# Kernel tuning notes

Hardware: AMD Instinct MI355X
Metric: run time of the kernel (lower is better)

The kernel has to match this reference:

```python
import jax, jax.numpy as jnp
import numpy as np
from jax import lax


def setup_inputs() -> dict:
    key = jax.random.key(0)
    ks = jax.random.split(key, 6)
    B, T, F, C = 32, 256, 64, 16
    CO, P, S, K = 16, 64, 32, 4
    x = jax.random.normal(ks[0], (B, T, F, C), dtype=jnp.float32)
    static = jax.random.normal(ks[1], (B, S), dtype=jnp.float32)
    conv_w = jax.random.normal(ks[2], (F, CO, C, K), dtype=jnp.float32) * (1.0 / np.sqrt(C * K))
    conv_b = jax.random.normal(ks[3], (F, CO), dtype=jnp.float32) * 0.01
    W_p = jax.random.normal(ks[4], (F * C + S, P), dtype=jnp.float32) * (1.0 / np.sqrt(F * C + S))
    b_p = jax.random.normal(ks[5], (P,), dtype=jnp.float32) * 0.01
    return {"x": x, "static": static, "conv_w": conv_w, "conv_b": conv_b,
            "W_p": W_p, "b_p": b_p, "dilation": 2}


def _tpc_forward(x, static, conv_w, conv_b, W_p, b_p, dilation):
    B, T, F, C = x.shape
    _, CO, _, K = conv_w.shape
    left_pad = dilation * (K - 1)
    # --- feature-wise causal temporal conv as one grouped dilated conv ---
    # [B, T, F, C] -> [B, F*C, T]  (NCH layout)
    xr = x.transpose(0, 2, 3, 1).reshape(B, F * C, T)
    kr = conv_w.reshape(F * CO, C, K)  # groups = F
    y = lax.conv_general_dilated(
        xr, kr,
        window_strides=(1,),
        padding=[(left_pad, 0)],  # causal left padding
        rhs_dilation=(dilation,),
        dimension_numbers=("NCH", "OIH", "NCH"),
        feature_group_count=F,
    )  # [B, F*CO, T]
    temp_out = y.reshape(B, F, CO, T).transpose(0, 3, 1, 2) + conv_b[None, None, :, :]
    # --- pointwise branch on flattened features + static ---
    flat_x = x.reshape(B, T, F * C)
    static_rep = jnp.broadcast_to(static[:, None, :], (B, T, static.shape[-1]))
    point_in = jnp.concatenate([flat_x, static_rep], axis=-1)  # [B, T, F*C+S]
    point_out = point_in @ W_p + b_p  # [B, T, P]
    point_bcast = jnp.broadcast_to(point_out[:, :, None, :], (B, T, F, point_out.shape[-1]))
    # --- concat fusion + ReLU ---
    fused = jnp.concatenate([x, temp_out, point_bcast], axis=-1)
    return jax.nn.relu(fused)


def reference(x, static, conv_w, conv_b, W_p, b_p, dilation):
    return _tpc_forward(x, static, conv_w, conv_b, W_p, b_p, dilation)
```

## Files before the change

kernel.cpp:

```cpp
#include <hip/hip_runtime.h>

#define B_  32
#define T_  256
#define F_  64
#define C_  16
#define CO_ 16
#define P_  64
#define S_  32
#define K_  4
#define FC_ 1024
#define OUTC 96
#define TT  8
#define NS  14

__global__ __launch_bounds__(512, 4) void tpc_fused(
    const float* __restrict__ x, const float* __restrict__ stat,
    const float* __restrict__ cw, const float* __restrict__ cb,
    const float* __restrict__ Wp, const float* __restrict__ bp,
    float* __restrict__ out)
{
    __shared__ __align__(16) float xs[NS * FC_];
    __shared__ __align__(16) float u[4096];

    int tid = threadIdx.x;
    int blk = blockIdx.x;
    int b  = blk >> 5;
    int t0 = (blk & 31) * TT;

    #pragma unroll
    for (int it = 0; it < 7; ++it) {
        int v = it * 512 + tid;
        int slice = v >> 8;
        int pos   = v & 255;
        int tg = t0 - 6 + slice;
        float4 val = make_float4(0.f, 0.f, 0.f, 0.f);
        if (tg >= 0)
            val = *(const float4*)(x + ((size_t)(b * T_ + tg)) * FC_ + pos * 4);
        *(float4*)(xs + slice * FC_ + pos * 4) = val;
    }
    __syncthreads();

    {
        int p  = tid & 63;
        int ks = tid >> 6;
        float acc[TT];
        #pragma unroll
        for (int r = 0; r < TT; ++r) acc[r] = 0.f;
        int k0base = ks * 128;
        for (int kk = 0; kk < 128; kk += 4) {
            int k0 = k0base + kk;
            float w0 = Wp[(size_t)(k0 + 0) * P_ + p];
            float w1 = Wp[(size_t)(k0 + 1) * P_ + p];
            float w2 = Wp[(size_t)(k0 + 2) * P_ + p];
            float w3 = Wp[(size_t)(k0 + 3) * P_ + p];
            #pragma unroll
            for (int r = 0; r < TT; ++r) {
                float4 xv = *(const float4*)(xs + (6 + r) * FC_ + k0);
                acc[r] += xv.x * w0 + xv.y * w1 + xv.z * w2 + xv.w * w3;
            }
        }
        #pragma unroll
        for (int r = 0; r < TT; ++r)
            u[(ks * TT + r) * P_ + p] = acc[r];
    }
    __syncthreads();

    {
        int p = tid & 63;
        int r = tid >> 6;
        float s = bp[p];
        const float* wst = Wp + (size_t)FC_ * P_;
        #pragma unroll 8
        for (int si = 0; si < S_; ++si)
            s += stat[b * S_ + si] * wst[si * P_ + p];
        #pragma unroll
        for (int ks = 0; ks < 8; ++ks)
            s += u[(ks * TT + r) * P_ + p];
        __syncthreads();
        u[3072 + r * P_ + p] = fmaxf(s, 0.f);
    }
    __syncthreads();

    int co = tid & 15;
    int fh = tid >> 4;
    int p  = tid & 63;
    int fg = tid >> 6;

    #pragma unroll
    for (int half = 0; half < 2; ++half) {
        int f = half * 32 + fh;
        float w[64];
        const float4* wg = (const float4*)(cw + ((size_t)(f * CO_ + co)) * (C_ * K_));
        #pragma unroll
        for (int j = 0; j < 16; ++j) {
            float4 t4 = wg[j];
            w[4 * j + 0] = t4.x; w[4 * j + 1] = t4.y;
            w[4 * j + 2] = t4.z; w[4 * j + 3] = t4.w;
        }
        float bias = cb[f * CO_ + co];

        for (int tl = 0; tl < TT; ++tl) {
            float temp = bias;
            #pragma unroll
            for (int k = 0; k < K_; ++k) {
                const float* sp = xs + (tl + 2 * k) * FC_ + f * C_;
                #pragma unroll
                for (int c4 = 0; c4 < 4; ++c4) {
                    float4 xv = *(const float4*)(sp + c4 * 4);
                    temp += xv.x * w[(c4 * 4 + 0) * 4 + k];
                    temp += xv.y * w[(c4 * 4 + 1) * 4 + k];
                    temp += xv.z * w[(c4 * 4 + 2) * 4 + k];
                    temp += xv.w * w[(c4 * 4 + 3) * 4 + k];
                }
            }
            u[fh * OUTC + 16 + co] = fmaxf(temp, 0.f);
            u[fh * OUTC + co] = fmaxf(xs[(tl + 6) * FC_ + f * C_ + co], 0.f);
            float pvv = u[3072 + tl * P_ + p];
            #pragma unroll
            for (int fo = 0; fo < 4; ++fo)
                u[(fo * 8 + fg) * OUTC + 32 + p] = pvv;

            asm volatile("s_waitcnt lgkmcnt(0)" ::: "memory");
            __builtin_amdgcn_sched_barrier(0);
            __builtin_amdgcn_s_barrier();
            __builtin_amdgcn_sched_barrier(0);

            {
                const float4* src = (const float4*)u;
                float4* dst = (float4*)(out + ((size_t)(b * T_ + t0 + tl)) * F_ * OUTC
                                        + half * 3072);
                dst[tid] = src[tid];
                if (tid < 256) dst[512 + tid] = src[512 + tid];
            }

            asm volatile("s_waitcnt lgkmcnt(0)" ::: "memory");
            __builtin_amdgcn_sched_barrier(0);
            __builtin_amdgcn_s_barrier();
            __builtin_amdgcn_sched_barrier(0);
        }
    }
}

extern "C" void kernel_launch(void* const* d_in, const int* in_sizes, int n_in,
                              void* d_out, int out_size, void* d_ws, size_t ws_size,
                              hipStream_t stream) {
    const float* x    = (const float*)d_in[0];
    const float* stat = (const float*)d_in[1];
    const float* cw   = (const float*)d_in[2];
    const float* cb   = (const float*)d_in[3];
    const float* Wp   = (const float*)d_in[4];
    const float* bp   = (const float*)d_in[5];
    float* out = (float*)d_out;

    tpc_fused<<<1024, 512, 0, stream>>>(x, stat, cw, cb, Wp, bp, out);
}
```

Before: 280.2 us.

## Read x from global instead of LDS and double-buffer the output staging

```diff
diff --git a/kernel.cpp b/kernel.cpp
--- a/kernel.cpp
+++ b/kernel.cpp
@@ -11,7 +11,6 @@
 #define FC_ 1024
 #define OUTC 96
 #define TT  8
-#define NS  14
 
 __global__ __launch_bounds__(512, 4) void tpc_fused(
     const float* __restrict__ x, const float* __restrict__ stat,
@@ -19,26 +18,16 @@
     const float* __restrict__ Wp, const float* __restrict__ bp,
     float* __restrict__ out)
 {
-    __shared__ __align__(16) float xs[NS * FC_];
-    __shared__ __align__(16) float u[4096];
+    __shared__ __align__(16) float lds[6656];
+    float* part = lds;
+    float* pv   = lds + 6144;
 
     int tid = threadIdx.x;
     int blk = blockIdx.x;
     int b  = blk >> 5;
     int t0 = (blk & 31) * TT;
 
-    #pragma unroll
-    for (int it = 0; it < 7; ++it) {
-        int v = it * 512 + tid;
-        int slice = v >> 8;
-        int pos   = v & 255;
-        int tg = t0 - 6 + slice;
-        float4 val = make_float4(0.f, 0.f, 0.f, 0.f);
-        if (tg >= 0)
-            val = *(const float4*)(x + ((size_t)(b * T_ + tg)) * FC_ + pos * 4);
-        *(float4*)(xs + slice * FC_ + pos * 4) = val;
-    }
-    __syncthreads();
+    const float* xrow0 = x + ((size_t)(b * T_ + t0)) * FC_;
 
     {
         int p  = tid & 63;
@@ -55,13 +44,13 @@
             float w3 = Wp[(size_t)(k0 + 3) * P_ + p];
             #pragma unroll
             for (int r = 0; r < TT; ++r) {
-                float4 xv = *(const float4*)(xs + (6 + r) * FC_ + k0);
+                float4 xv = *(const float4*)(xrow0 + r * FC_ + k0);
                 acc[r] += xv.x * w0 + xv.y * w1 + xv.z * w2 + xv.w * w3;
             }
         }
         #pragma unroll
         for (int r = 0; r < TT; ++r)
-            u[(ks * TT + r) * P_ + p] = acc[r];
+            part[(ks * TT + r) * P_ + p] = acc[r];
     }
     __syncthreads();
 
@@ -75,9 +64,8 @@
             s += stat[b * S_ + si] * wst[si * P_ + p];
         #pragma unroll
         for (int ks = 0; ks < 8; ++ks)
-            s += u[(ks * TT + r) * P_ + p];
-        __syncthreads();
-        u[3072 + r * P_ + p] = fmaxf(s, 0.f);
+            s += part[(ks * TT + r) * P_ + p];
+        pv[r * P_ + p] = fmaxf(s, 0.f);
     }
     __syncthreads();
 
@@ -86,6 +74,7 @@
     int p  = tid & 63;
     int fg = tid >> 6;
 
+    int bufsel = 0;
     #pragma unroll
     for (int half = 0; half < 2; ++half) {
         int f = half * 32 + fh;
@@ -100,25 +89,30 @@
         float bias = cb[f * CO_ + co];
 
         for (int tl = 0; tl < TT; ++tl) {
+            float* st = lds + bufsel * 3072;
             float temp = bias;
             #pragma unroll
             for (int k = 0; k < K_; ++k) {
-                const float* sp = xs + (tl + 2 * k) * FC_ + f * C_;
-                #pragma unroll
-                for (int c4 = 0; c4 < 4; ++c4) {
-                    float4 xv = *(const float4*)(sp + c4 * 4);
-                    temp += xv.x * w[(c4 * 4 + 0) * 4 + k];
-                    temp += xv.y * w[(c4 * 4 + 1) * 4 + k];
-                    temp += xv.z * w[(c4 * 4 + 2) * 4 + k];
-                    temp += xv.w * w[(c4 * 4 + 3) * 4 + k];
+                int tg = t0 + tl + 2 * k - 6;
+                if (tg >= 0) {
+                    const float* sp = x + ((size_t)(b * T_ + tg)) * FC_ + f * C_;
+                    #pragma unroll
+                    for (int c4 = 0; c4 < 4; ++c4) {
+                        float4 xv = *(const float4*)(sp + c4 * 4);
+                        temp += xv.x * w[(c4 * 4 + 0) * 4 + k];
+                        temp += xv.y * w[(c4 * 4 + 1) * 4 + k];
+                        temp += xv.z * w[(c4 * 4 + 2) * 4 + k];
+                        temp += xv.w * w[(c4 * 4 + 3) * 4 + k];
+                    }
                 }
             }
-            u[fh * OUTC + 16 + co] = fmaxf(temp, 0.f);
-            u[fh * OUTC + co] = fmaxf(xs[(tl + 6) * FC_ + f * C_ + co], 0.f);
-            float pvv = u[3072 + tl * P_ + p];
+            st[fh * OUTC + 16 + co] = fmaxf(temp, 0.f);
+            st[fh * OUTC + co] =
+                fmaxf(x[((size_t)(b * T_ + t0 + tl)) * FC_ + f * C_ + co], 0.f);
+            float pvv = pv[tl * P_ + p];
             #pragma unroll
             for (int fo = 0; fo < 4; ++fo)
-                u[(fo * 8 + fg) * OUTC + 32 + p] = pvv;
+                st[(fo * 8 + fg) * OUTC + 32 + p] = pvv;
 
             asm volatile("s_waitcnt lgkmcnt(0)" ::: "memory");
             __builtin_amdgcn_sched_barrier(0);
@@ -126,17 +120,13 @@
             __builtin_amdgcn_sched_barrier(0);
 
             {
-                const float4* src = (const float4*)u;
+                const float4* src = (const float4*)st;
                 float4* dst = (float4*)(out + ((size_t)(b * T_ + t0 + tl)) * F_ * OUTC
                                         + half * 3072);
                 dst[tid] = src[tid];
                 if (tid < 256) dst[512 + tid] = src[512 + tid];
             }
-
-            asm volatile("s_waitcnt lgkmcnt(0)" ::: "memory");
-            __builtin_amdgcn_sched_barrier(0);
-            __builtin_amdgcn_s_barrier();
-            __builtin_amdgcn_sched_barrier(0);
+            bufsel ^= 1;
         }
     }
 }
```

Measured after the change: 382.1 us. 1.36x slower.

## Split pointwise projection into separate kernel writing workspace before fused output kernel

Applied to the files above, without the earlier changes.

```diff
diff --git a/kernel.cpp b/kernel.cpp
--- a/kernel.cpp
+++ b/kernel.cpp
@@ -12,15 +12,73 @@
 #define OUTC 96
 #define TT  8
 #define NS  14
+#define TA  16
 
-__global__ __launch_bounds__(512, 4) void tpc_fused(
+
+__global__ __launch_bounds__(512, 4) void tpc_point(
     const float* __restrict__ x, const float* __restrict__ stat,
-    const float* __restrict__ cw, const float* __restrict__ cb,
     const float* __restrict__ Wp, const float* __restrict__ bp,
+    float* __restrict__ pvg)
+{
+    __shared__ float part[8 * TA * P_];
+
+    int tid = threadIdx.x;
+    int blk = blockIdx.x;
+    int b  = blk >> 4;
+    int t0 = (blk & 15) * TA;
+
+    int p  = tid & 63;
+    int ks = tid >> 6;
+    const float* xbase = x + ((size_t)(b * T_ + t0)) * FC_;
+
+    float acc[TA];
+    #pragma unroll
+    for (int r = 0; r < TA; ++r) acc[r] = 0.f;
+
+    int k0b = ks * 128;
+    for (int kk = 0; kk < 128; kk += 4) {
+        int k0 = k0b + kk;
+        float w0 = Wp[(size_t)(k0 + 0) * P_ + p];
+        float w1 = Wp[(size_t)(k0 + 1) * P_ + p];
+        float w2 = Wp[(size_t)(k0 + 2) * P_ + p];
+        float w3 = Wp[(size_t)(k0 + 3) * P_ + p];
+        #pragma unroll
+        for (int r = 0; r < TA; ++r) {
+            float4 xv = *(const float4*)(xbase + r * FC_ + k0);
+            acc[r] += xv.x * w0 + xv.y * w1 + xv.z * w2 + xv.w * w3;
+        }
+    }
+    #pragma unroll
+    for (int r = 0; r < TA; ++r)
+        part[(ks * TA + r) * P_ + p] = acc[r];
+    __syncthreads();
+
+    {
+        int rr = tid >> 6;
+        float s0 = bp[p];
+        const float* wst = Wp + (size_t)FC_ * P_;
+        #pragma unroll 8
+        for (int si = 0; si < S_; ++si)
+            s0 += stat[b * S_ + si] * wst[si * P_ + p];
+        #pragma unroll
+        for (int h = 0; h < 2; ++h) {
+            int r = rr + h * 8;
+            float s = s0;
+            #pragma unroll
+            for (int k2 = 0; k2 < 8; ++k2)
+                s += part[(k2 * TA + r) * P_ + p];
+            pvg[((size_t)(b * T_ + t0 + r)) * P_ + p] = fmaxf(s, 0.f);
+        }
+    }
+}
+
+__global__ __launch_bounds__(512, 4) void tpc_fuse(
+    const float* __restrict__ x, const float* __restrict__ cw,
+    const float* __restrict__ cb, const float* __restrict__ pvg,
     float* __restrict__ out)
 {
     __shared__ __align__(16) float xs[NS * FC_];
-    __shared__ __align__(16) float u[4096];
+    __shared__ __align__(16) float u[3072];
 
     int tid = threadIdx.x;
     int blk = blockIdx.x;
@@ -38,52 +96,17 @@
             val = *(const float4*)(x + ((size_t)(b * T_ + tg)) * FC_ + pos * 4);
         *(float4*)(xs + slice * FC_ + pos * 4) = val;
     }
-    __syncthreads();
 
-    {
-        int p  = tid & 63;
-        int ks = tid >> 6;
-        float acc[TT];
-        #pragma unroll
-        for (int r = 0; r < TT; ++r) acc[r] = 0.f;
-        int k0base = ks * 128;
-        for (int kk = 0; kk < 128; kk += 4) {
-            int k0 = k0base + kk;
-            float w0 = Wp[(size_t)(k0 + 0) * P_ + p];
-            float w1 = Wp[(size_t)(k0 + 1) * P_ + p];
-            float w2 = Wp[(size_t)(k0 + 2) * P_ + p];
-            float w3 = Wp[(size_t)(k0 + 3) * P_ + p];
-            #pragma unroll
-            for (int r = 0; r < TT; ++r) {
-                float4 xv = *(const float4*)(xs + (6 + r) * FC_ + k0);
-                acc[r] += xv.x * w0 + xv.y * w1 + xv.z * w2 + xv.w * w3;
-            }
-        }
-        #pragma unroll
-        for (int r = 0; r < TT; ++r)
-            u[(ks * TT + r) * P_ + p] = acc[r];
-    }
-    __syncthreads();
+    int p  = tid & 63;
+    float pvr[TT];
+    #pragma unroll
+    for (int tl = 0; tl < TT; ++tl)
+        pvr[tl] = pvg[((size_t)(b * T_ + t0 + tl)) * P_ + p];
 
-    {
-        int p = tid & 63;
-        int r = tid >> 6;
-        float s = bp[p];
-        const float* wst = Wp + (size_t)FC_ * P_;
-        #pragma unroll 8
-        for (int si = 0; si < S_; ++si)
-            s += stat[b * S_ + si] * wst[si * P_ + p];
-        #pragma unroll
-        for (int ks = 0; ks < 8; ++ks)
-            s += u[(ks * TT + r) * P_ + p];
-        __syncthreads();
-        u[3072 + r * P_ + p] = fmaxf(s, 0.f);
-    }
     __syncthreads();
 
     int co = tid & 15;
     int fh = tid >> 4;
-    int p  = tid & 63;
     int fg = tid >> 6;
 
     #pragma unroll
@@ -115,7 +138,7 @@
             }
             u[fh * OUTC + 16 + co] = fmaxf(temp, 0.f);
             u[fh * OUTC + co] = fmaxf(xs[(tl + 6) * FC_ + f * C_ + co], 0.f);
-            float pvv = u[3072 + tl * P_ + p];
+            float pvv = pvr[tl];
             #pragma unroll
             for (int fo = 0; fo < 4; ++fo)
                 u[(fo * 8 + fg) * OUTC + 32 + p] = pvv;
@@ -151,6 +174,8 @@
     const float* Wp   = (const float*)d_in[4];
     const float* bp   = (const float*)d_in[5];
     float* out = (float*)d_out;
+    float* pvg = (float*)d_ws;
 
-    tpc_fused<<<1024, 512, 0, stream>>>(x, stat, cw, cb, Wp, bp, out);
+    tpc_point<<<512, 512, 0, stream>>>(x, stat, Wp, bp, pvg);
+    tpc_fuse<<<1024, 512, 0, stream>>>(x, cw, cb, pvg, out);
 }
```

After: 329.3 us. +17.5%, slower.

## Compute all conv outputs into registers, then stage full rows with double-buffered LDS

Applied to the files above, without the earlier changes.

```diff
diff --git a/kernel.cpp b/kernel.cpp
--- a/kernel.cpp
+++ b/kernel.cpp
@@ -19,8 +19,10 @@
     const float* __restrict__ Wp, const float* __restrict__ bp,
     float* __restrict__ out)
 {
-    __shared__ __align__(16) float xs[NS * FC_];
-    __shared__ __align__(16) float u[4096];
+    __shared__ __align__(16) float lds[18944];
+    float* xs   = lds;
+    float* part = lds + 14336;
+    float* pv   = lds + 18432;
 
     int tid = threadIdx.x;
     int blk = blockIdx.x;
@@ -61,12 +63,16 @@
         }
         #pragma unroll
         for (int r = 0; r < TT; ++r)
-            u[(ks * TT + r) * P_ + p] = acc[r];
+            part[(ks * TT + r) * P_ + p] = acc[r];
     }
     __syncthreads();
 
+    int p  = tid & 63;
+    int co = tid & 15;
+    int fh = tid >> 4;
+    int fg = tid >> 6;
+
     {
-        int p = tid & 63;
         int r = tid >> 6;
         float s = bp[p];
         const float* wst = Wp + (size_t)FC_ * P_;
@@ -75,17 +81,11 @@
             s += stat[b * S_ + si] * wst[si * P_ + p];
         #pragma unroll
         for (int ks = 0; ks < 8; ++ks)
-            s += u[(ks * TT + r) * P_ + p];
-        __syncthreads();
-        u[3072 + r * P_ + p] = fmaxf(s, 0.f);
+            s += part[(ks * TT + r) * P_ + p];
+        pv[r * P_ + p] = fmaxf(s, 0.f);
     }
-    __syncthreads();
 
-    int co = tid & 15;
-    int fh = tid >> 4;
-    int p  = tid & 63;
-    int fg = tid >> 6;
-
+    float cv[2][TT], px[2][TT];
     #pragma unroll
     for (int half = 0; half < 2; ++half) {
         int f = half * 32 + fh;
@@ -98,7 +98,7 @@
             w[4 * j + 2] = t4.z; w[4 * j + 3] = t4.w;
         }
         float bias = cb[f * CO_ + co];
-
+        #pragma unroll
         for (int tl = 0; tl < TT; ++tl) {
             float temp = bias;
             #pragma unroll
@@ -113,31 +113,38 @@
                     temp += xv.w * w[(c4 * 4 + 3) * 4 + k];
                 }
             }
-            u[fh * OUTC + 16 + co] = fmaxf(temp, 0.f);
-            u[fh * OUTC + co] = fmaxf(xs[(tl + 6) * FC_ + f * C_ + co], 0.f);
-            float pvv = u[3072 + tl * P_ + p];
-            #pragma unroll
-            for (int fo = 0; fo < 4; ++fo)
-                u[(fo * 8 + fg) * OUTC + 32 + p] = pvv;
+            cv[half][tl] = fmaxf(temp, 0.f);
+            px[half][tl] = fmaxf(xs[(tl + 6) * FC_ + f * C_ + co], 0.f);
+        }
+    }
+    __syncthreads();
 
-            asm volatile("s_waitcnt lgkmcnt(0)" ::: "memory");
-            __builtin_amdgcn_sched_barrier(0);
-            __builtin_amdgcn_s_barrier();
-            __builtin_amdgcn_sched_barrier(0);
+    float pvr[TT];
+    #pragma unroll
+    for (int tl = 0; tl < TT; ++tl)
+        pvr[tl] = pv[tl * P_ + p];
 
-            {
-                const float4* src = (const float4*)u;
-                float4* dst = (float4*)(out + ((size_t)(b * T_ + t0 + tl)) * F_ * OUTC
-                                        + half * 3072);
-                dst[tid] = src[tid];
-                if (tid < 256) dst[512 + tid] = src[512 + tid];
-            }
+    for (int tl = 0; tl < TT; ++tl) {
+        float* st = lds + (tl & 1) * 6144;
+        st[fh * OUTC + co]               = px[0][tl];
+        st[fh * OUTC + 16 + co]          = cv[0][tl];
+        st[(fh + 32) * OUTC + co]        = px[1][tl];
+        st[(fh + 32) * OUTC + 16 + co]   = cv[1][tl];
+        float pvv = pvr[tl];
+        #pragma unroll
+        for (int fo = 0; fo < 8; ++fo)
+            st[(fo * 8 + fg) * OUTC + 32 + p] = pvv;
 
-            asm volatile("s_waitcnt lgkmcnt(0)" ::: "memory");
-            __builtin_amdgcn_sched_barrier(0);
-            __builtin_amdgcn_s_barrier();
-            __builtin_amdgcn_sched_barrier(0);
-        }
+        asm volatile("s_waitcnt lgkmcnt(0)" ::: "memory");
+        __builtin_amdgcn_sched_barrier(0);
+        __builtin_amdgcn_s_barrier();
+        __builtin_amdgcn_sched_barrier(0);
+
+        const float4* src = (const float4*)st;
+        float4* dst = (float4*)(out + ((size_t)(b * T_ + t0 + tl)) * F_ * OUTC);
+        dst[tid]        = src[tid];
+        dst[512 + tid]  = src[512 + tid];
+        dst[1024 + tid] = src[1024 + tid];
     }
 }
 
```

New measurement: 273.7 us. 2.3% less time.
